# Optimization experiments

Hardware: AMD Instinct MI355X
Metric: run time of the kernel (lower is better)

## Reference

```python
import jax, jax.numpy as jnp
import numpy as np

# Hyperparameters mirroring init_kwargs
MAX_ITERS = 100      # ADMM outer iterations
RHO = 1.0            # ADMM penalty
INNER = 20           # PGD steps per x-subproblem
STEP = 5e-05         # fixed PGD step (x_inner_step given, so no svdvals branch)


def setup_inputs() -> dict:
    key = jax.random.key(0)
    kA, kb, kc = jax.random.split(key, 3)
    m, n = 2048, 4096
    A = jax.random.normal(kA, (m, n), dtype=jnp.float32)
    b = jax.random.uniform(kb, (m,), dtype=jnp.float32)
    c = jax.random.uniform(kc, (n,), dtype=jnp.float32)
    return {"A": A, "b": b, "c": c}


def _admm(A, b, c):
    m, n = A.shape

    def outer(carry, _):
        x, s, u = carry
        r = s + b - u  # target for the x-subproblem residual

        # PGD on: min_{x>=0} c^T x + (rho/2)||A x - r||^2
        def pgd(x, _):
            g = c + RHO * (A.T @ (A @ x - r))
            return jnp.maximum(x - STEP * g, 0.0), None

        x, _ = jax.lax.scan(pgd, x, None, length=INNER)

        Ax = A @ x
        s = jnp.maximum(Ax - b + u, 0.0)   # slack update (projection onto >=0)
        u = u + (Ax - s - b)               # scaled dual update
        return (x, s, u), None

    init = (jnp.zeros((n,), A.dtype), jnp.zeros((m,), A.dtype), jnp.zeros((m,), A.dtype))
    (x, s, u), _ = jax.lax.scan(outer, init, None, length=MAX_ITERS)
    lambda_kkt = -RHO * u
    return x, s, u, lambda_kkt


def reference(A, b, c):
    # return_history=False -> torch module returns (x, s, u, lambda_kkt, None);
    # we return the 4 tensor outputs.
    return _admm(A, b, c)
```

## Files before the change

### kernel.cpp

```cpp
#include <hip/hip_runtime.h>
#include <hip/hip_cooperative_groups.h>

namespace cg = cooperative_groups;

#define M_ROWS 2048
#define N_COLS 4096
#define RHO_C 1.0f
#define STEP_C 5e-05f
#define MAX_ITERS_C 100
#define INNER_C 20

__device__ __forceinline__ float aload(const float* p) {
    return __hip_atomic_load(p, __ATOMIC_RELAXED, __HIP_MEMORY_SCOPE_AGENT);
}
__device__ __forceinline__ void astore(float* p, float v) {
    __hip_atomic_store(p, v, __ATOMIC_RELAXED, __HIP_MEMORY_SCOPE_AGENT);
}
__device__ __forceinline__ float2 aload2(const float* p) {
    unsigned long long v = __hip_atomic_load(
        (const unsigned long long*)p, __ATOMIC_RELAXED,
        __HIP_MEMORY_SCOPE_AGENT);
    union { unsigned long long u; float2 f; } c; c.u = v; return c.f;
}

__device__ inline void fast_barrier(unsigned* bs, int blk, unsigned n) {
    __syncthreads();
    if (threadIdx.x == 0) {
        __builtin_amdgcn_fence(__ATOMIC_RELEASE, "workgroup");
        unsigned* leaf = bs + ((blk & 7) << 5);
        unsigned* root = bs + 256;
        unsigned* ep   = bs + 288;
        unsigned old = __hip_atomic_fetch_add(leaf, 1u, __ATOMIC_RELAXED,
                                              __HIP_MEMORY_SCOPE_AGENT);
        if (old == n * 32u + 31u) {
            unsigned ro = __hip_atomic_fetch_add(root, 1u, __ATOMIC_RELAXED,
                                                 __HIP_MEMORY_SCOPE_AGENT);
            if (ro == n * 8u + 7u)
                __hip_atomic_fetch_add(ep, 1u, __ATOMIC_RELAXED,
                                       __HIP_MEMORY_SCOPE_AGENT);
        }
        while (__hip_atomic_load(ep, __ATOMIC_RELAXED,
                                 __HIP_MEMORY_SCOPE_AGENT) <= n)
            __builtin_amdgcn_s_sleep(1);
        __builtin_amdgcn_fence(__ATOMIC_ACQUIRE, "workgroup");
    }
    __syncthreads();
}

__global__ __launch_bounds__(1024) void admm_gram(
    const float* __restrict__ A, const float* __restrict__ bvec,
    const float* __restrict__ cvec, float* __restrict__ out,
    float* __restrict__ x0, float* __restrict__ x1,
    float* __restrict__ rt, unsigned* __restrict__ bstate)
{
    cg::grid_group grid = cg::this_grid();
    const int tid  = threadIdx.x;
    const int blk  = blockIdx.x;
    const int lane = tid & 63;
    const int wave = tid >> 6;
    const int cgp  = wave >> 2;
    const int rq   = wave & 3;

    __shared__ float  abuf[4 * N_COLS];
    __shared__ float4 xs4[1024];
    __shared__ float  red[4][16];
    __shared__ float4 gred[64];
    __shared__ float  wl[16], cw[16];
    __shared__ float  sv[8], uv[8], tpart[16];

    float* xs = reinterpret_cast<float*>(xs4);
    const float4* A4 = reinterpret_cast<const float4*>(A);
    float4* abuf4 = reinterpret_cast<float4*>(abuf);

    if (tid < 16) {
        cw[tid] = cvec[blk * 16 + tid];
        astore(&x0[blk * 16 + tid], 0.0f);
    }
    if (tid < 8) {
        sv[tid] = 0.0f; uv[tid] = 0.0f;
        astore(&rt[blk * 8 + tid], bvec[blk * 8 + tid]);
    }
    if (blk == 0 && tid < 320) bstate[tid] = 0u;

    float accM[4][16];
    #pragma unroll
    for (int r = 0; r < 4; ++r)
        #pragma unroll
        for (int k = 0; k < 16; ++k) accM[r][k] = 0.0f;

    for (int i0 = 0; i0 < M_ROWS; i0 += 4) {
        #pragma unroll
        for (int ii = 0; ii < 4; ++ii)
            abuf4[ii * 1024 + tid] = A4[(size_t)(i0 + ii) * 1024 + tid];
        __syncthreads();
        #pragma unroll
        for (int ii = 0; ii < 4; ++ii) {
            const float*  row  = abuf + ii * N_COLS;
            const float4* row4 = abuf4 + ii * 1024;
            float4 av[4];
            #pragma unroll
            for (int q = 0; q < 4; ++q)
                av[q] = row4[256 * cgp + 64 * q + lane];
            float cb[4];
            #pragma unroll
            for (int r = 0; r < 4; ++r) cb[r] = row[blk * 16 + rq * 4 + r];
            #pragma unroll
            for (int r = 0; r < 4; ++r)
                #pragma unroll
                for (int q = 0; q < 4; ++q) {
                    accM[r][4 * q + 0] = fmaf(cb[r], av[q].x, accM[r][4 * q + 0]);
                    accM[r][4 * q + 1] = fmaf(cb[r], av[q].y, accM[r][4 * q + 1]);
                    accM[r][4 * q + 2] = fmaf(cb[r], av[q].z, accM[r][4 * q + 2]);
                    accM[r][4 * q + 3] = fmaf(cb[r], av[q].w, accM[r][4 * q + 3]);
                }
        }
        __syncthreads();
    }

    grid.sync();
    unsigned bar_n = 0;

    for (int outer = 0; outer < MAX_ITERS_C; ++outer) {
        abuf[tid]        = aload(&rt[tid]);
        abuf[tid + 1024] = aload(&rt[tid + 1024]);
        __syncthreads();
        {
            const int p = tid >> 2, gq = tid & 3;
            float4 acc = {0.f, 0.f, 0.f, 0.f};
            #pragma unroll
            for (int k2 = 0; k2 < 8; ++k2) {
                const int i = p + 256 * k2;
                const float tv = abuf[i];
                float4 a = A4[(size_t)i * 1024 + blk * 4 + gq];
                acc.x = fmaf(a.x, tv, acc.x); acc.y = fmaf(a.y, tv, acc.y);
                acc.z = fmaf(a.z, tv, acc.z); acc.w = fmaf(a.w, tv, acc.w);
            }
            #pragma unroll
            for (int off = 4; off < 64; off <<= 1) {
                acc.x += __shfl_xor(acc.x, off);
                acc.y += __shfl_xor(acc.y, off);
                acc.z += __shfl_xor(acc.z, off);
                acc.w += __shfl_xor(acc.w, off);
            }
            if ((lane >> 2) == 0) gred[wave * 4 + gq] = acc;
        }
        __syncthreads();
        if (tid < 4) {
            float4 tot = {0.f, 0.f, 0.f, 0.f};
            #pragma unroll
            for (int w = 0; w < 16; ++w) {
                float4 v = gred[w * 4 + tid];
                tot.x += v.x; tot.y += v.y; tot.z += v.z; tot.w += v.w;
            }
            wl[tid * 4 + 0] = tot.x; wl[tid * 4 + 1] = tot.y;
            wl[tid * 4 + 2] = tot.z; wl[tid * 4 + 3] = tot.w;
        }
        __syncthreads();

        for (int inner = 0; inner < INNER_C; ++inner) {
            const float* xsrc = (inner & 1) ? x1 : x0;
            float*       xdst = (inner & 1) ? x0 : x1;

            {
                float2 lo = aload2(xsrc + 4 * tid);
                float2 hi = aload2(xsrc + 4 * tid + 2);
                xs4[tid] = make_float4(lo.x, lo.y, hi.x, hi.y);
            }
            __syncthreads();

            float4 xq[4];
            #pragma unroll
            for (int q = 0; q < 4; ++q)
                xq[q] = xs4[256 * cgp + 64 * q + lane];

            float4 pd = {0.f, 0.f, 0.f, 0.f};
            #pragma unroll
            for (int q = 0; q < 4; ++q) {
                pd.x = fmaf(accM[0][4*q+0], xq[q].x, pd.x);
                pd.x = fmaf(accM[0][4*q+1], xq[q].y, pd.x);
                pd.x = fmaf(accM[0][4*q+2], xq[q].z, pd.x);
                pd.x = fmaf(accM[0][4*q+3], xq[q].w, pd.x);
                pd.y = fmaf(accM[1][4*q+0], xq[q].x, pd.y);
                pd.y = fmaf(accM[1][4*q+1], xq[q].y, pd.y);
                pd.y = fmaf(accM[1][4*q+2], xq[q].z, pd.y);
                pd.y = fmaf(accM[1][4*q+3], xq[q].w, pd.y);
                pd.z = fmaf(accM[2][4*q+0], xq[q].x, pd.z);
                pd.z = fmaf(accM[2][4*q+1], xq[q].y, pd.z);
                pd.z = fmaf(accM[2][4*q+2], xq[q].z, pd.z);
                pd.z = fmaf(accM[2][4*q+3], xq[q].w, pd.z);
                pd.w = fmaf(accM[3][4*q+0], xq[q].x, pd.w);
                pd.w = fmaf(accM[3][4*q+1], xq[q].y, pd.w);
                pd.w = fmaf(accM[3][4*q+2], xq[q].z, pd.w);
                pd.w = fmaf(accM[3][4*q+3], xq[q].w, pd.w);
            }

            #pragma unroll
            for (int off = 32; off; off >>= 1) {
                pd.x += __shfl_xor(pd.x, off);
                pd.y += __shfl_xor(pd.y, off);
                pd.z += __shfl_xor(pd.z, off);
                pd.w += __shfl_xor(pd.w, off);
            }
            if (lane == 0) {
                red[cgp][rq * 4 + 0] = pd.x;
                red[cgp][rq * 4 + 1] = pd.y;
                red[cgp][rq * 4 + 2] = pd.z;
                red[cgp][rq * 4 + 3] = pd.w;
            }
            __syncthreads();

            if (tid < 16) {
                const float y = red[0][tid] + red[1][tid]
                              + red[2][tid] + red[3][tid];
                const float g = cw[tid] + RHO_C * (y - wl[tid]);
                float xn = xs[blk * 16 + tid] - STEP_C * g;
                xn = xn > 0.f ? xn : 0.f;
                astore(&xdst[blk * 16 + tid], xn);
            }
            fast_barrier(bstate, blk, bar_n); ++bar_n;
        }

        {
            float2 lo = aload2(x0 + 4 * tid);
            float2 hi = aload2(x0 + 4 * tid + 2);
            xs4[tid] = make_float4(lo.x, lo.y, hi.x, hi.y);
        }
        __syncthreads();
        {
            const int r = blk * 8 + (wave >> 1), h = wave & 1;
            const float4* Ar = A4 + (size_t)r * 1024 + h * 512;
            const float4* xh = xs4 + h * 512;
            float4 acc = {0.f, 0.f, 0.f, 0.f};
            #pragma unroll
            for (int it = 0; it < 8; ++it) {
                float4 a = Ar[it * 64 + lane], xv = xh[it * 64 + lane];
                acc.x = fmaf(a.x, xv.x, acc.x); acc.y = fmaf(a.y, xv.y, acc.y);
                acc.z = fmaf(a.z, xv.z, acc.z); acc.w = fmaf(a.w, xv.w, acc.w);
            }
            float d = acc.x + acc.y + acc.z + acc.w;
            #pragma unroll
            for (int off = 32; off; off >>= 1) d += __shfl_xor(d, off);
            if (lane == 0) tpart[wave] = d;
        }
        __syncthreads();
        if (tid < 8) {
            const int i = blk * 8 + tid;
            const float a  = tpart[2 * tid] + tpart[2 * tid + 1];
            const float bb = bvec[i];
            const float uu = uv[tid];
            float sn = a - bb + uu; sn = sn > 0.f ? sn : 0.f;
            const float un = uu + a - sn - bb;
            sv[tid] = sn; uv[tid] = un;
            astore(&rt[i], sn + bb - un);
        }
        fast_barrier(bstate, blk, bar_n); ++bar_n;
    }

    if (tid < 16) out[blk * 16 + tid] = aload(&x0[blk * 16 + tid]);
    if (tid < 8) {
        const int i = blk * 8 + tid;
        out[4096 + i] = sv[tid];
        out[6144 + i] = uv[tid];
        out[8192 + i] = -uv[tid];
    }
}

extern "C" void kernel_launch(void* const* d_in, const int* in_sizes, int n_in,
                              void* d_out, int out_size, void* d_ws, size_t ws_size,
                              hipStream_t stream) {
    const float* A    = (const float*)d_in[0];
    const float* bvec = (const float*)d_in[1];
    const float* cvec = (const float*)d_in[2];
    float* out = (float*)d_out;

    float* ws = (float*)d_ws;
    float* x0 = ws;
    float* x1 = ws + 4096;
    float* rt = ws + 8192;
    unsigned* bstate = (unsigned*)(ws + 12288);

    void* args[] = { (void*)&A, (void*)&bvec, (void*)&cvec, (void*)&out,
                     (void*)&x0, (void*)&x1, (void*)&rt, (void*)&bstate };
    hipError_t err = hipLaunchCooperativeKernel((const void*)admm_gram,
                               dim3(256), dim3(1024), args, 0, stream);
    (void)err;
}
```

Baseline: 10.89 ms.

## Replace grid barriers with tagged dataflow flags packed beside x and r values

Removes the hierarchical atomic grid barrier used after every inner PGD step and every outer iteration. Each x and r element is now stored as a 64-bit word holding the value and an iteration tag, and consumers spin until every word they read carries the expected tag. Each block can then start as soon as its own inputs are ready, with no global rendezvous. The costs are doubled bytes for x and r traffic and polling on many words instead of one counter. Correctness depends on double-buffer reuse being safe without a barrier.

```diff
diff --git a/kernel.cpp b/kernel.cpp
--- a/kernel.cpp
+++ b/kernel.cpp
@@ -10,48 +10,45 @@
 #define MAX_ITERS_C 100
 #define INNER_C 20
 
-__device__ __forceinline__ float aload(const float* p) {
+__device__ __forceinline__ unsigned long long ald64(const unsigned long long* p) {
     return __hip_atomic_load(p, __ATOMIC_RELAXED, __HIP_MEMORY_SCOPE_AGENT);
 }
-__device__ __forceinline__ void astore(float* p, float v) {
+__device__ __forceinline__ void ast64(unsigned long long* p, unsigned long long v) {
     __hip_atomic_store(p, v, __ATOMIC_RELAXED, __HIP_MEMORY_SCOPE_AGENT);
 }
-__device__ __forceinline__ float2 aload2(const float* p) {
-    unsigned long long v = __hip_atomic_load(
-        (const unsigned long long*)p, __ATOMIC_RELAXED,
-        __HIP_MEMORY_SCOPE_AGENT);
-    union { unsigned long long u; float2 f; } c; c.u = v; return c.f;
-}
-
-__device__ inline void fast_barrier(unsigned* bs, int blk, unsigned n) {
+__device__ __forceinline__ unsigned long long packf(float f, unsigned tag) {
+    union { float f; unsigned u; } c; c.f = f;
+    return ((unsigned long long)tag << 32) | (unsigned long long)c.u;
+}
+__device__ __forceinline__ float unpackf(unsigned long long v) {
+    union { unsigned u; float f; } c; c.u = (unsigned)v; return c.f;
+}
+
+#define STAGE_X(TAG)                                                         \
+    {                                                                        \
+        const unsigned long long* xp =                                       \
+            xP + ((((unsigned)(TAG)) & 1u) << 12) + ((unsigned)tid << 2);    \
+        unsigned long long w0, w1, w2, w3;                                   \
+        for (;;) {                                                           \
+            w0 = ald64(xp + 0); w1 = ald64(xp + 1);                          \
+            w2 = ald64(xp + 2); w3 = ald64(xp + 3);                          \
+            unsigned mm = ((unsigned)(w0 >> 32) ^ (unsigned)(TAG))           \
+                        | ((unsigned)(w1 >> 32) ^ (unsigned)(TAG))           \
+                        | ((unsigned)(w2 >> 32) ^ (unsigned)(TAG))           \
+                        | ((unsigned)(w3 >> 32) ^ (unsigned)(TAG));          \
+            if (mm == 0u) break;                                             \
+            __builtin_amdgcn_s_sleep(1);                                     \
+        }                                                                    \
+        xs4[tid] = make_float4(unpackf(w0), unpackf(w1),                     \
+                               unpackf(w2), unpackf(w3));                    \
+    }                                                                        \
     __syncthreads();
-    if (threadIdx.x == 0) {
-        __builtin_amdgcn_fence(__ATOMIC_RELEASE, "workgroup");
-        unsigned* leaf = bs + ((blk & 7) << 5);
-        unsigned* root = bs + 256;
-        unsigned* ep   = bs + 288;
-        unsigned old = __hip_atomic_fetch_add(leaf, 1u, __ATOMIC_RELAXED,
-                                              __HIP_MEMORY_SCOPE_AGENT);
-        if (old == n * 32u + 31u) {
-            unsigned ro = __hip_atomic_fetch_add(root, 1u, __ATOMIC_RELAXED,
-                                                 __HIP_MEMORY_SCOPE_AGENT);
-            if (ro == n * 8u + 7u)
-                __hip_atomic_fetch_add(ep, 1u, __ATOMIC_RELAXED,
-                                       __HIP_MEMORY_SCOPE_AGENT);
-        }
-        while (__hip_atomic_load(ep, __ATOMIC_RELAXED,
-                                 __HIP_MEMORY_SCOPE_AGENT) <= n)
-            __builtin_amdgcn_s_sleep(1);
-        __builtin_amdgcn_fence(__ATOMIC_ACQUIRE, "workgroup");
-    }
-    __syncthreads();
-}
-
-__global__ __launch_bounds__(1024) void admm_gram(
+
+__global__ __launch_bounds__(1024) void admm_df(
     const float* __restrict__ A, const float* __restrict__ bvec,
     const float* __restrict__ cvec, float* __restrict__ out,
-    float* __restrict__ x0, float* __restrict__ x1,
-    float* __restrict__ rt, unsigned* __restrict__ bstate)
+    unsigned long long* __restrict__ xP,
+    unsigned long long* __restrict__ rtP)
 {
     cg::grid_group grid = cg::this_grid();
     const int tid  = threadIdx.x;
@@ -74,13 +71,13 @@
 
     if (tid < 16) {
         cw[tid] = cvec[blk * 16 + tid];
-        astore(&x0[blk * 16 + tid], 0.0f);
+        ast64(&xP[blk * 16 + tid],        packf(0.0f, 0u));
+        ast64(&xP[4096 + blk * 16 + tid], packf(0.0f, 0xFFFFFFFFu));
     }
     if (tid < 8) {
         sv[tid] = 0.0f; uv[tid] = 0.0f;
-        astore(&rt[blk * 8 + tid], bvec[blk * 8 + tid]);
-    }
-    if (blk == 0 && tid < 320) bstate[tid] = 0u;
+        ast64(&rtP[blk * 8 + tid], packf(bvec[blk * 8 + tid], 0u));
+    }
 
     float accM[4][16];
     #pragma unroll
@@ -118,11 +115,24 @@
     }
 
     grid.sync();
-    unsigned bar_n = 0;
+
+    unsigned t = 0;
+    STAGE_X(0u)
 
     for (int outer = 0; outer < MAX_ITERS_C; ++outer) {
-        abuf[tid]        = aload(&rt[tid]);
-        abuf[tid + 1024] = aload(&rt[tid + 1024]);
+        {
+            const unsigned long long* rp = rtP + tid;
+            unsigned long long wa, wb;
+            for (;;) {
+                wa = ald64(rp); wb = ald64(rp + 1024);
+                unsigned mm = ((unsigned)(wa >> 32) ^ (unsigned)outer)
+                            | ((unsigned)(wb >> 32) ^ (unsigned)outer);
+                if (mm == 0u) break;
+                __builtin_amdgcn_s_sleep(1);
+            }
+            abuf[tid]        = unpackf(wa);
+            abuf[tid + 1024] = unpackf(wb);
+        }
         __syncthreads();
         {
             const int p = tid >> 2, gq = tid & 3;
@@ -158,15 +168,7 @@
         __syncthreads();
 
         for (int inner = 0; inner < INNER_C; ++inner) {
-            const float* xsrc = (inner & 1) ? x1 : x0;
-            float*       xdst = (inner & 1) ? x0 : x1;
-
-            {
-                float2 lo = aload2(xsrc + 4 * tid);
-                float2 hi = aload2(xsrc + 4 * tid + 2);
-                xs4[tid] = make_float4(lo.x, lo.y, hi.x, hi.y);
-            }
-            __syncthreads();
+            if (inner != 0) { STAGE_X(t) }
 
             float4 xq[4];
             #pragma unroll
@@ -215,17 +217,13 @@
                 const float g = cw[tid] + RHO_C * (y - wl[tid]);
                 float xn = xs[blk * 16 + tid] - STEP_C * g;
                 xn = xn > 0.f ? xn : 0.f;
-                astore(&xdst[blk * 16 + tid], xn);
-            }
-            fast_barrier(bstate, blk, bar_n); ++bar_n;
-        }
-
-        {
-            float2 lo = aload2(x0 + 4 * tid);
-            float2 hi = aload2(x0 + 4 * tid + 2);
-            xs4[tid] = make_float4(lo.x, lo.y, hi.x, hi.y);
-        }
-        __syncthreads();
+                ast64(&xP[(((t + 1u) & 1u) << 12) + blk * 16 + tid],
+                      packf(xn, t + 1u));
+            }
+            ++t;
+        }
+
+        STAGE_X(t)
         {
             const int r = blk * 8 + (wave >> 1), h = wave & 1;
             const float4* Ar = A4 + (size_t)r * 1024 + h * 512;
@@ -251,12 +249,11 @@
             float sn = a - bb + uu; sn = sn > 0.f ? sn : 0.f;
             const float un = uu + a - sn - bb;
             sv[tid] = sn; uv[tid] = un;
-            astore(&rt[i], sn + bb - un);
-        }
-        fast_barrier(bstate, blk, bar_n); ++bar_n;
-    }
-
-    if (tid < 16) out[blk * 16 + tid] = aload(&x0[blk * 16 + tid]);
+            ast64(&rtP[i], packf(sn + bb - un, (unsigned)outer + 1u));
+        }
+    }
+
+    if (tid < 16) out[blk * 16 + tid] = xs[blk * 16 + tid];
     if (tid < 8) {
         const int i = blk * 8 + tid;
         out[4096 + i] = sv[tid];
@@ -273,15 +270,12 @@
     const float* cvec = (const float*)d_in[2];
     float* out = (float*)d_out;
 
-    float* ws = (float*)d_ws;
-    float* x0 = ws;
-    float* x1 = ws + 4096;
-    float* rt = ws + 8192;
-    unsigned* bstate = (unsigned*)(ws + 12288);
+    unsigned long long* xP  = (unsigned long long*)d_ws;
+    unsigned long long* rtP = xP + 2 * 4096;
 
     void* args[] = { (void*)&A, (void*)&bvec, (void*)&cvec, (void*)&out,
-                     (void*)&x0, (void*)&x1, (void*)&rt, (void*)&bstate };
-    hipError_t err = hipLaunchCooperativeKernel((const void*)admm_gram,
+                     (void*)&xP, (void*)&rtP };
+    hipError_t err = hipLaunchCooperativeKernel((const void*)admm_df,
                                dim3(256), dim3(1024), args, 0, stream);
     (void)err;
 }
```

New measurement: 12.52 ms. 1.15x slower.
